# Kernel optimization log

Measured on AMD Instinct MI355X. Metric: run time of the kernel, lower is better.

The kernel has to match this reference:

```python
import jax, jax.numpy as jnp
import numpy as np


def _log_g(x):
    # log of g(x) = where(x>=0, x+0.5, sigmoid(x)), computed stably in log-space
    return jnp.where(x >= 0, jnp.log(jax.nn.relu(x) + 0.5), -jax.nn.softplus(-x))


def _mingru_layer(h, w_hg_l, w_out_l, rms_w_l):
    # h: [B,T,H]; w_hg_l: [2*DI,H]; w_out_l: [H,DI]; rms_w_l: [H]
    hg = jnp.einsum('bth,dh->btd', h, w_hg_l)          # [B,T,2*DI]
    hidden, gate = jnp.split(hg, 2, axis=-1)            # each [B,T,DI]
    log_coeffs = -jax.nn.softplus(gate)                 # log a_t
    log_values = -jax.nn.softplus(-gate) + _log_g(hidden)  # log(z_t * g(h~_t))
    # Heinsen log-space associative scan (prev_hidden = 0, contributes nothing)
    a_star = jnp.cumsum(log_coeffs, axis=1)
    log_h = a_star + jax.lax.cumlogsumexp(log_values - a_star, axis=1)
    out = jnp.exp(log_h)                                # [B,T,DI]
    out = jnp.einsum('btd,hd->bth', out, w_out_l) + h   # proj_out + residual
    eps = jnp.finfo(out.dtype).eps
    out = out * jax.lax.rsqrt(jnp.mean(out * out, axis=-1, keepdims=True) + eps)
    return out * rms_w_l


def setup_inputs() -> dict:
    key = jax.random.key(0)
    ks = jax.random.split(key, 6)
    B, T, OBS, H, DI, L, A = 32, 1024, 512, 512, 1024, 2, 16
    s = 0.05  # weight scale keeps softplus/exp chain well-conditioned
    return {
        'x': jax.random.normal(ks[0], (B, T, OBS), jnp.float32),
        'enc_w': s * jax.random.normal(ks[1], (H, OBS), jnp.float32),
        'enc_b': jnp.zeros((H,), jnp.float32),
        'w_hg': s * jax.random.normal(ks[2], (L, 2 * DI, H), jnp.float32),
        'w_out': s * jax.random.normal(ks[3], (L, H, DI), jnp.float32),
        'rms_w': jnp.ones((L, H), jnp.float32),
        'dec_w': s * jax.random.normal(ks[4], (A, H), jnp.float32),
        'dec_b': jnp.zeros((A,), jnp.float32),
        'val_w': s * jax.random.normal(ks[5], (1, H), jnp.float32),
        'val_b': jnp.zeros((1,), jnp.float32),
    }


def reference(x, enc_w, enc_b, w_hg, w_out, rms_w, dec_w, dec_b, val_w, val_b):
    B, T, _ = x.shape
    # encoder: Linear + exact gelu
    h = jax.nn.gelu(jnp.einsum('bto,ho->bth', x, enc_w) + enc_b, approximate=False)
    for l in range(w_hg.shape[0]):
        h = _mingru_layer(h, w_hg[l], w_out[l], rms_w[l])
    flat = h.reshape(B * T, -1)
    logits = flat @ dec_w.T + dec_b                     # [B*T, A]
    values = (flat @ val_w.T + val_b).reshape(B, T)
    return logits, values
```

## Files before the change

### kernel.cpp

```cpp
#include <hip/hip_runtime.h>
#include <math.h>

#define MROWS 32768
#define T_LEN 1024

typedef __attribute__((ext_vector_type(8))) short bf16x8;
typedef __attribute__((ext_vector_type(4))) float f32x4;

__device__ __forceinline__ unsigned short f2bf(float f) {
  union { float f; unsigned u; } x; x.f = f;
  unsigned r = x.u + 0x7fffu + ((x.u >> 16) & 1u);
  return (unsigned short)(r >> 16);
}
__device__ __forceinline__ float bf2f(unsigned short u) {
  union { unsigned u; float f; } x; x.u = ((unsigned)u) << 16; return x.f;
}

__device__ __forceinline__ void gload_lds16(const void* g, void* l) {
  __builtin_amdgcn_global_load_lds(
      (const __attribute__((address_space(1))) void*)g,
      (__attribute__((address_space(3))) void*)l, 16, 0, 0);
}

template<int MODE>
__global__ __launch_bounds__(256, 2)
void gemm_bt(const unsigned short* __restrict__ A, int lda,
             const unsigned short* __restrict__ B,
             int N, int K,
             const float* __restrict__ bias,
             const unsigned short* res,
             unsigned short* outb)
{
  __shared__ __align__(16) unsigned short sA[128 * 64];
  __shared__ __align__(16) unsigned short sB[128 * 64];
  const int tid  = threadIdx.x;
  const int wave = tid >> 6, lane = tid & 63;
  const int m0 = blockIdx.x * 128, n0 = blockIdx.y * 128;
  const int srow   = lane >> 3;
  const int sslotb = ((lane & 7) ^ srow) * 16;
  const int wm = wave & 1, wn = wave >> 1;
  const int r16 = lane & 15, q = lane >> 4;

  f32x4 acc[4][4];
#pragma unroll
  for (int i = 0; i < 4; i++)
#pragma unroll
    for (int j = 0; j < 4; j++)
#pragma unroll
      for (int e = 0; e < 4; e++) acc[i][j][e] = 0.0f;

  const char* Ab = (const char*)A;
  const char* Bb = (const char*)B;
  char* sAb = (char*)sA;
  char* sBb = (char*)sB;

  for (int kt = 0; kt < K; kt += 64) {
#pragma unroll
    for (int i = 0; i < 4; i++) {
      const int j = wave * 4 + i;
      const int row = j * 8 + srow;
      gload_lds16(Ab + ((size_t)(m0 + row) * lda + kt) * 2 + sslotb, sAb + j * 1024);
      gload_lds16(Bb + ((size_t)(n0 + row) * K   + kt) * 2 + sslotb, sBb + j * 1024);
    }
    __syncthreads();
#pragma unroll
    for (int kh = 0; kh < 2; kh++) {
      bf16x8 af[4], bfr[4];
#pragma unroll
      for (int mt = 0; mt < 4; mt++) {
        const int row = wm * 64 + mt * 16 + r16;
        af[mt] = *(const bf16x8*)(sAb + row * 128 + ((((kh << 2) | q) ^ (row & 7)) * 16));
      }
#pragma unroll
      for (int nt = 0; nt < 4; nt++) {
        const int row = wn * 64 + nt * 16 + r16;
        bfr[nt] = *(const bf16x8*)(sBb + row * 128 + ((((kh << 2) | q) ^ (row & 7)) * 16));
      }
#pragma unroll
      for (int mt = 0; mt < 4; mt++)
#pragma unroll
        for (int nt = 0; nt < 4; nt++)
          acc[mt][nt] = __builtin_amdgcn_mfma_f32_16x16x32_bf16(af[mt], bfr[nt], acc[mt][nt], 0, 0, 0);
    }
    __syncthreads();
  }

#pragma unroll
  for (int mt = 0; mt < 4; mt++) {
#pragma unroll
    for (int nt = 0; nt < 4; nt++) {
#pragma unroll
      for (int r = 0; r < 4; r++) {
        const int m = m0 + wm * 64 + mt * 16 + q * 4 + r;
        const int n = n0 + wn * 64 + nt * 16 + r16;
        const size_t idx = (size_t)m * N + n;
        float v = acc[mt][nt][r];
        if (MODE == 0) {
          v += bias[n];
          v = 0.5f * v * (1.0f + erff(v * 0.70710678118654752f));
        } else if (MODE == 2) {
          v += bf2f(res[idx]);
        }
        outb[idx] = f2bf(v);
      }
    }
  }
}

__global__ __launch_bounds__(256)
void scan_kernel(unsigned short* hg) {
  __shared__ unsigned long long sAB[256 * 16];
  __shared__ float sA[16 * 32];
  __shared__ float sH[16 * 32];
  const int b  = blockIdx.x >> 5;
  const int dg = blockIdx.x & 31;
  const int tid = threadIdx.x;
  const int c  = tid >> 4;
  const int dp = tid & 15;
  unsigned int* base = (unsigned int*)(hg + (size_t)b * T_LEN * 2048);
  const int du = dg * 16 + dp;

  float carry = 0.0f;

  for (int seg = 0; seg < 4; ++seg) {
    const int t0 = seg * 256 + c * 16;

    float A0 = 1.0f, A1 = 1.0f, h0 = 0.0f, h1 = 0.0f;
#pragma unroll
    for (int tl = 0; tl < 16; ++tl) {
      const int t = t0 + tl;
      const unsigned hidp = base[t * 1024 + du];
      const unsigned gtp  = base[t * 1024 + 512 + du];
      const float hid0 = bf2f((unsigned short)hidp), hid1 = bf2f((unsigned short)(hidp >> 16));
      const float gt0  = bf2f((unsigned short)gtp),  gt1  = bf2f((unsigned short)(gtp >> 16));
      const float e0 = __expf(-gt0), e1 = __expf(-gt1);
      const float r0 = 1.0f / (1.0f + e0), r1 = 1.0f / (1.0f + e1);
      const float g0 = (hid0 >= 0.0f) ? (hid0 + 0.5f) : (1.0f / (1.0f + __expf(-hid0)));
      const float g1 = (hid1 >= 0.0f) ? (hid1 + 0.5f) : (1.0f / (1.0f + __expf(-hid1)));
      const unsigned short ra0 = f2bf(e0 * r0), rb0 = f2bf(r0 * g0);
      const unsigned short ra1 = f2bf(e1 * r1), rb1 = f2bf(r1 * g1);
      sAB[(c * 16 + tl) * 16 + dp] =
          (unsigned long long)((unsigned)ra0 | ((unsigned)ra1 << 16)) |
          ((unsigned long long)((unsigned)rb0 | ((unsigned)rb1 << 16)) << 32);
      const float fa0 = bf2f(ra0), fb0 = bf2f(rb0), fa1 = bf2f(ra1), fb1 = bf2f(rb1);
      A0 *= fa0; h0 = fa0 * h0 + fb0;
      A1 *= fa1; h1 = fa1 * h1 + fb1;
    }
    sA[c * 32 + 2 * dp] = A0;  sA[c * 32 + 2 * dp + 1] = A1;
    sH[c * 32 + 2 * dp] = h0;  sH[c * 32 + 2 * dp + 1] = h1;
    __syncthreads();

    if (tid < 32) {
      float hin = carry;
#pragma unroll
      for (int cc = 0; cc < 16; ++cc) {
        const float a  = sA[cc * 32 + tid];
        const float hs = sH[cc * 32 + tid];
        sA[cc * 32 + tid] = hin;
        hin = hs + a * hin;
      }
      carry = hin;
    }
    __syncthreads();

    float hh0 = sA[c * 32 + 2 * dp];
    float hh1 = sA[c * 32 + 2 * dp + 1];
#pragma unroll
    for (int tl = 0; tl < 16; ++tl) {
      const int t = t0 + tl;
      const unsigned long long ab = sAB[(c * 16 + tl) * 16 + dp];
      const float fa0 = bf2f((unsigned short)ab);
      const float fa1 = bf2f((unsigned short)(ab >> 16));
      const float fb0 = bf2f((unsigned short)(ab >> 32));
      const float fb1 = bf2f((unsigned short)(ab >> 48));
      hh0 = fa0 * hh0 + fb0;
      hh1 = fa1 * hh1 + fb1;
      base[t * 1024 + 512 + du] = (unsigned)f2bf(hh0) | ((unsigned)f2bf(hh1) << 16);
    }
    __syncthreads();
  }
}

__global__ __launch_bounds__(256)
void rms_kernel(unsigned short* __restrict__ hb, const float* __restrict__ w) {
  const int wid  = (blockIdx.x * blockDim.x + threadIdx.x) >> 6;
  const int lane = threadIdx.x & 63;
  unsigned short* row = hb + (size_t)wid * 512;
  float v[8];
  float ss = 0.0f;
#pragma unroll
  for (int j = 0; j < 8; j++) { v[j] = bf2f(row[lane + 64 * j]); ss += v[j] * v[j]; }
#pragma unroll
  for (int off = 32; off >= 1; off >>= 1) ss += __shfl_xor(ss, off, 64);
  const float r = rsqrtf(ss * (1.0f / 512.0f) + 1.1920929e-7f);
#pragma unroll
  for (int j = 0; j < 8; j++) {
    const int k = lane + 64 * j;
    row[k] = f2bf(v[j] * r * w[k]);
  }
}

__global__ __launch_bounds__(256)
void decoder_kernel(const unsigned short* __restrict__ hb,
                    const float* __restrict__ dec_w,
                    const float* __restrict__ dec_b,
                    const float* __restrict__ val_w,
                    const float* __restrict__ val_b,
                    float* __restrict__ out) {
  const int nw   = (gridDim.x * blockDim.x) >> 6;
  const int wid  = (blockIdx.x * blockDim.x + threadIdx.x) >> 6;
  const int lane = threadIdx.x & 63;
  float* logits = out;
  float* values = out + (size_t)MROWS * 16;
  for (int row = wid; row < MROWS; row += nw) {
    const unsigned short* hr = hb + (size_t)row * 512;
    float acc[17];
#pragma unroll
    for (int a = 0; a < 17; a++) acc[a] = 0.0f;
#pragma unroll
    for (int j = 0; j < 8; j++) {
      const int k = lane + 64 * j;
      const float hv = bf2f(hr[k]);
#pragma unroll
      for (int a = 0; a < 16; a++) acc[a] += hv * dec_w[a * 512 + k];
      acc[16] += hv * val_w[k];
    }
#pragma unroll
    for (int a = 0; a < 17; a++) {
#pragma unroll
      for (int off = 32; off >= 1; off >>= 1) acc[a] += __shfl_xor(acc[a], off, 64);
    }
    if (lane == 0) {
#pragma unroll
      for (int a = 0; a < 16; a++) logits[(size_t)row * 16 + a] = acc[a] + dec_b[a];
      values[row] = acc[16] + val_b[0];
    }
  }
}

__global__ __launch_bounds__(256)
void conv_bf16(const float* __restrict__ in, unsigned short* __restrict__ out, int n4) {
  const int i = blockIdx.x * blockDim.x + threadIdx.x;
  if (i < n4) {
    const float4 v = ((const float4*)in)[i];
    const unsigned long long pack =
        (unsigned long long)f2bf(v.x) |
        ((unsigned long long)f2bf(v.y) << 16) |
        ((unsigned long long)f2bf(v.z) << 32) |
        ((unsigned long long)f2bf(v.w) << 48);
    ((unsigned long long*)out)[i] = pack;
  }
}

extern "C" void kernel_launch(void* const* d_in, const int* in_sizes, int n_in,
                              void* d_out, int out_size, void* d_ws, size_t ws_size,
                              hipStream_t stream) {
  const float* x     = (const float*)d_in[0];
  const float* enc_w = (const float*)d_in[1];
  const float* enc_b = (const float*)d_in[2];
  const float* w_hg  = (const float*)d_in[3];
  const float* w_out = (const float*)d_in[4];
  const float* rms_w = (const float*)d_in[5];
  const float* dec_w = (const float*)d_in[6];
  const float* dec_b = (const float*)d_in[7];
  const float* val_w = (const float*)d_in[8];
  const float* val_b = (const float*)d_in[9];
  float* out = (float*)d_out;

  if (ws_size < 174587904u) return;

  char* ws = (char*)d_ws;
  unsigned short* hg   = (unsigned short*)(ws);
  unsigned short* xb   = (unsigned short*)(ws);
  unsigned short* hb   = (unsigned short*)(ws + 134217728);
  unsigned short* wenc = (unsigned short*)(ws + 167772160);
  unsigned short* whg  = wenc + 262144;
  unsigned short* wout = whg + 2097152;

  conv_bf16<<<16384, 256, 0, stream>>>(x, xb, 4194304);
  conv_bf16<<<256,   256, 0, stream>>>(enc_w, wenc, 65536);
  conv_bf16<<<2048,  256, 0, stream>>>(w_hg, whg, 524288);
  conv_bf16<<<1024,  256, 0, stream>>>(w_out, wout, 262144);

  gemm_bt<0><<<dim3(256, 4), 256, 0, stream>>>(xb, 512, wenc, 512, 512, enc_b, nullptr, hb);

  for (int l = 0; l < 2; ++l) {
    gemm_bt<1><<<dim3(256, 16), 256, 0, stream>>>(hb, 512, whg + (size_t)l * 1048576, 2048, 512,
                                                  nullptr, nullptr, hg);
    scan_kernel<<<1024, 256, 0, stream>>>(hg);
    gemm_bt<2><<<dim3(256, 4), 256, 0, stream>>>(hg + 1024, 2048, wout + (size_t)l * 524288,
                                                 512, 1024, nullptr, hb, hb);
    rms_kernel<<<8192, 256, 0, stream>>>(hb, rms_w + (size_t)l * 512);
  }

  decoder_kernel<<<512, 256, 0, stream>>>(hb, dec_w, dec_b, val_w, val_b, out);
}
```

Measured before the change: 617.7 us.

## Rewrite bf16 GEMM with 256x256 tiles, 4-stage LDS pipeline and XCD swizzle

The GEMM kernel moves from 128x128 tiles with 256 threads and a single-buffered K=64 loop to 256x256 tiles with 512 threads. It uses a four-buffer, K=32-step LDS ring with explicit vmcnt waits so that global-to-LDS loads for the next three steps overlap the MFMA work on the current one. A 1D grid is remapped with a modulo-8 swizzle so neighbouring blocks share A/B tiles within an XCD. MFMA sections also raise wave priority. The cost is 128 KB of LDS per block, which allows only one block per CU, plus 128 accumulator registers per thread. The swizzle also assumes the block count is divisible by 8 and that M is exactly 128 tiles.

```diff
diff --git a/kernel.cpp b/kernel.cpp
--- a/kernel.cpp
+++ b/kernel.cpp
@@ -3,6 +3,7 @@
 
 #define MROWS 32768
 #define T_LEN 1024
+#define MT 128
 
 typedef __attribute__((ext_vector_type(8))) short bf16x8;
 typedef __attribute__((ext_vector_type(4))) float f32x4;
@@ -23,7 +24,7 @@
 }
 
 template<int MODE>
-__global__ __launch_bounds__(256, 2)
+__global__ __launch_bounds__(512, 2)
 void gemm_bt(const unsigned short* __restrict__ A, int lda,
              const unsigned short* __restrict__ B,
              int N, int K,
@@ -31,67 +32,90 @@
              const unsigned short* res,
              unsigned short* outb)
 {
-  __shared__ __align__(16) unsigned short sA[128 * 64];
-  __shared__ __align__(16) unsigned short sB[128 * 64];
+  __shared__ __align__(16) char smem[131072];
+  char* sAb = smem;
+  char* sBb = smem + 65536;
+
   const int tid  = threadIdx.x;
   const int wave = tid >> 6, lane = tid & 63;
-  const int m0 = blockIdx.x * 128, n0 = blockIdx.y * 128;
-  const int srow   = lane >> 3;
-  const int sslotb = ((lane & 7) ^ srow) * 16;
-  const int wm = wave & 1, wn = wave >> 1;
+
+  const int nwg = gridDim.x;
+  const int lid = blockIdx.x;
+  const int swz = (lid & 7) * (nwg >> 3) + (lid >> 3);
+  const int m0 = (swz & (MT - 1)) << 8;
+  const int n0 = (swz >> 7) << 8;
+
+  const int wm = wave >> 2, wn = wave & 3;
   const int r16 = lane & 15, q = lane >> 4;
 
-  f32x4 acc[4][4];
-#pragma unroll
-  for (int i = 0; i < 4; i++)
-#pragma unroll
-    for (int j = 0; j < 4; j++)
-#pragma unroll
-      for (int e = 0; e < 4; e++) acc[i][j][e] = 0.0f;
+  const int srow = lane >> 2;
+  const int xl   = (srow & 3) ^ ((srow >> 2) & 3);
+  const int cgb  = ((lane & 3) ^ xl) * 16;
+  const int rdswz = ((q ^ (r16 & 3) ^ ((r16 >> 2) & 3)) * 16);
+  const int aoff = wm * 8192 + r16 * 64 + rdswz;
+  const int boff = wn * 4096 + r16 * 64 + rdswz;
 
   const char* Ab = (const char*)A;
   const char* Bb = (const char*)B;
-  char* sAb = (char*)sA;
-  char* sBb = (char*)sB;
-
-  for (int kt = 0; kt < K; kt += 64) {
-#pragma unroll
-    for (int i = 0; i < 4; i++) {
-      const int j = wave * 4 + i;
-      const int row = j * 8 + srow;
-      gload_lds16(Ab + ((size_t)(m0 + row) * lda + kt) * 2 + sslotb, sAb + j * 1024);
-      gload_lds16(Bb + ((size_t)(n0 + row) * K   + kt) * 2 + sslotb, sBb + j * 1024);
-    }
-    __syncthreads();
-#pragma unroll
-    for (int kh = 0; kh < 2; kh++) {
-      bf16x8 af[4], bfr[4];
-#pragma unroll
-      for (int mt = 0; mt < 4; mt++) {
-        const int row = wm * 64 + mt * 16 + r16;
-        af[mt] = *(const bf16x8*)(sAb + row * 128 + ((((kh << 2) | q) ^ (row & 7)) * 16));
-      }
-#pragma unroll
-      for (int nt = 0; nt < 4; nt++) {
-        const int row = wn * 64 + nt * 16 + r16;
-        bfr[nt] = *(const bf16x8*)(sBb + row * 128 + ((((kh << 2) | q) ^ (row & 7)) * 16));
-      }
-#pragma unroll
-      for (int mt = 0; mt < 4; mt++)
-#pragma unroll
-        for (int nt = 0; nt < 4; nt++)
-          acc[mt][nt] = __builtin_amdgcn_mfma_f32_16x16x32_bf16(af[mt], bfr[nt], acc[mt][nt], 0, 0, 0);
-    }
-    __syncthreads();
-  }
-
-#pragma unroll
-  for (int mt = 0; mt < 4; mt++) {
-#pragma unroll
-    for (int nt = 0; nt < 4; nt++) {
-#pragma unroll
-      for (int r = 0; r < 4; r++) {
-        const int m = m0 + wm * 64 + mt * 16 + q * 4 + r;
+  const int NT = K >> 5;
+
+  f32x4 acc[8][4];
+#pragma unroll
+  for (int i = 0; i < 8; i++)
+#pragma unroll
+    for (int j = 0; j < 4; j++)
+#pragma unroll
+      for (int e = 0; e < 4; e++) acc[i][j][e] = 0.0f;
+
+  auto stage = [&](int u) {
+    const int buf = u & 3;
+    const int kt  = u << 5;
+    char* dA = sAb + buf * 16384;
+    char* dB = sBb + buf * 16384;
+#pragma unroll
+    for (int i = 0; i < 2; ++i) {
+      const int j = wave * 2 + i;
+      const int r = j * 16 + srow;
+      gload_lds16(Ab + ((size_t)(m0 + r) * lda + kt) * 2 + cgb, dA + j * 1024);
+      gload_lds16(Bb + ((size_t)(n0 + r) * K   + kt) * 2 + cgb, dB + j * 1024);
+    }
+  };
+
+  stage(0); stage(1); stage(2);
+
+  for (int u = 0; u < NT; ++u) {
+    if (u + 2 < NT)      asm volatile("s_waitcnt vmcnt(8)" ::: "memory");
+    else if (u + 1 < NT) asm volatile("s_waitcnt vmcnt(4)" ::: "memory");
+    else                 asm volatile("s_waitcnt vmcnt(0)" ::: "memory");
+    __builtin_amdgcn_s_barrier();
+    asm volatile("" ::: "memory");
+
+    if (u + 3 < NT) stage(u + 3);
+
+    const char* bufA = sAb + (u & 3) * 16384;
+    const char* bufB = sBb + (u & 3) * 16384;
+    bf16x8 bfr[4];
+#pragma unroll
+    for (int nt = 0; nt < 4; ++nt)
+      bfr[nt] = *(const bf16x8*)(bufB + boff + nt * 1024);
+    __builtin_amdgcn_s_setprio(1);
+#pragma unroll
+    for (int mt = 0; mt < 8; ++mt) {
+      const bf16x8 af = *(const bf16x8*)(bufA + aoff + mt * 1024);
+#pragma unroll
+      for (int nt = 0; nt < 4; ++nt)
+        acc[mt][nt] = __builtin_amdgcn_mfma_f32_16x16x32_bf16(af, bfr[nt], acc[mt][nt], 0, 0, 0);
+    }
+    __builtin_amdgcn_s_setprio(0);
+  }
+
+#pragma unroll
+  for (int mt = 0; mt < 8; ++mt) {
+#pragma unroll
+    for (int nt = 0; nt < 4; ++nt) {
+#pragma unroll
+      for (int r = 0; r < 4; ++r) {
+        const int m = m0 + wm * 128 + mt * 16 + q * 4 + r;
         const int n = n0 + wn * 64 + nt * 16 + r16;
         const size_t idx = (size_t)m * N + n;
         float v = acc[mt][nt][r];
@@ -282,14 +306,14 @@
   conv_bf16<<<2048,  256, 0, stream>>>(w_hg, whg, 524288);
   conv_bf16<<<1024,  256, 0, stream>>>(w_out, wout, 262144);
 
-  gemm_bt<0><<<dim3(256, 4), 256, 0, stream>>>(xb, 512, wenc, 512, 512, enc_b, nullptr, hb);
+  gemm_bt<0><<<256, 512, 0, stream>>>(xb, 512, wenc, 512, 512, enc_b, nullptr, hb);
 
   for (int l = 0; l < 2; ++l) {
-    gemm_bt<1><<<dim3(256, 16), 256, 0, stream>>>(hb, 512, whg + (size_t)l * 1048576, 2048, 512,
-                                                  nullptr, nullptr, hg);
+    gemm_bt<1><<<1024, 512, 0, stream>>>(hb, 512, whg + (size_t)l * 1048576, 2048, 512,
+                                         nullptr, nullptr, hg);
     scan_kernel<<<1024, 256, 0, stream>>>(hg);
-    gemm_bt<2><<<dim3(256, 4), 256, 0, stream>>>(hg + 1024, 2048, wout + (size_t)l * 524288,
-                                                 512, 1024, nullptr, hb, hb);
+    gemm_bt<2><<<256, 512, 0, stream>>>(hg + 1024, 2048, wout + (size_t)l * 524288,
+                                        512, 1024, nullptr, hb, hb);
     rms_kernel<<<8192, 256, 0, stream>>>(hb, rms_w + (size_t)l * 512);
   }
 
```

Result: slower. 680.5 us (+10.2%).
